# Optimization experiments

Measured on AMD Instinct MI355X. Metric: run time of the kernel, lower is better.

## Reference

```python
import jax, jax.numpy as jnp
import numpy as np

K = 3          # kernel size
KF = K * K     # kernel field = 9
PAD = 1
STRIDE = 1


def _conv(x, w, b):
    y = jax.lax.conv_general_dilated(
        x, w, (STRIDE, STRIDE), [(PAD, PAD), (PAD, PAD)],
        dimension_numbers=('NCHW', 'OIHW', 'NCHW'))
    return y + b[None, :, None, None]


def _bilinear_gather(x, py, px):
    # x: [B,C,H,W]; py/px: [B,KF,Ho,Wo] float sampling coords (zero-pad outside)
    B, C, H, W = x.shape
    xf = x.reshape(B, C, H * W)
    y0 = jnp.floor(py)
    x0 = jnp.floor(px)

    def corner(yc, xc):
        wy = 1.0 - jnp.abs(py - yc)
        wx = 1.0 - jnp.abs(px - xc)
        valid = (yc >= 0) & (yc <= H - 1) & (xc >= 0) & (xc <= W - 1)
        yi = jnp.clip(yc, 0, H - 1).astype(jnp.int32)
        xi = jnp.clip(xc, 0, W - 1).astype(jnp.int32)
        idx = (yi * W + xi).reshape(B, -1)               # [B, KF*Ho*Wo]
        v = jax.vmap(lambda f, i: f[:, i])(xf, idx)      # [B, C, KF*Ho*Wo]
        wgt = (wy * wx * valid.astype(x.dtype)).reshape(B, 1, -1)
        return v * wgt

    return (corner(y0, x0) + corner(y0, x0 + 1) +
            corner(y0 + 1, x0) + corner(y0 + 1, x0 + 1))  # [B,C,KF*Ho*Wo]


def _deform_conv(x, offset, mask, w, b):
    # modulated deformable conv v2 (mmcv offset layout: [y,x] interleaved per kernel pt)
    B, C, H, W = x.shape
    Ho, Wo = mask.shape[2], mask.shape[3]
    kh, kw = jnp.meshgrid(jnp.arange(K), jnp.arange(K), indexing='ij')
    kh = kh.reshape(-1).astype(x.dtype)   # [KF]
    kw = kw.reshape(-1).astype(x.dtype)
    base_y = (jnp.arange(Ho) * STRIDE - PAD).astype(x.dtype)
    base_x = (jnp.arange(Wo) * STRIDE - PAD).astype(x.dtype)
    off = offset.reshape(B, KF, 2, Ho, Wo)
    py = base_y[None, None, :, None] + kh[None, :, None, None] + off[:, :, 0]
    px = base_x[None, None, None, :] + kw[None, :, None, None] + off[:, :, 1]
    val = _bilinear_gather(x, py, px).reshape(B, C, KF, Ho, Wo)
    val = val * mask[:, None]                             # modulate
    out = jnp.einsum('bckhw,ock->bohw', val, w.reshape(w.shape[0], C, KF))
    return out + b[None, :, None, None]


def setup_inputs() -> dict:
    key = jax.random.key(0)
    k1, k2, k3 = jax.random.split(key, 3)
    B, C, H, W = 8, 64, 128, 128
    x = jax.random.normal(k1, (B, C, H, W), dtype=jnp.float32)
    w_om = jax.random.normal(k2, (3 * KF, C, K, K), dtype=jnp.float32) * 0.02
    b_om = jnp.zeros((3 * KF,), dtype=jnp.float32)
    w_dc = jax.random.normal(k3, (64, C, K, K), dtype=jnp.float32) * 0.05
    b_dc = jnp.zeros((64,), dtype=jnp.float32)
    return {"x": x, "w_om": w_om, "b_om": b_om, "w_dc": w_dc, "b_dc": b_dc}


def reference(x, w_om, b_om, w_dc, b_dc):
    om = _conv(x, w_om, b_om)                 # [B, 3*KF, H, W]
    offset = om[:, :2 * KF]
    mask = 2.0 * jax.nn.sigmoid(om[:, 2 * KF:])
    return _deform_conv(x, offset, mask, w_dc, b_dc)
```

## Files before the change

kernel.cpp:

```cpp
#include <hip/hip_runtime.h>
#include <cmath>

#define IH 128
#define IW 128
#define NB 8

typedef __attribute__((ext_vector_type(8))) short bf16x8;
typedef __attribute__((ext_vector_type(4))) float f32x4;

union U4B8 { uint4 u; bf16x8 h; };

#define OFFM_OFF 0
#define XT_OFF   3538944
#define WTDC_OFF (3538944 + 4194304)
#define WTOM_OFF (3538944 + 4194304 + 18432)

__device__ __forceinline__ unsigned short f32_to_bf16(float f) {
    unsigned int u = __float_as_uint(f);
    u += 0x7fffu + ((u >> 16) & 1u);
    return (unsigned short)(u >> 16);
}

__global__ void transpose_weights(const float* __restrict__ w_dc,
                                  const float* __restrict__ w_om,
                                  unsigned short* __restrict__ wt_dc16,
                                  unsigned short* __restrict__ wt_om16) {
    int idx = blockIdx.x * blockDim.x + threadIdx.x;
    if (idx < 9 * 64 * 64) {
        int k = idx >> 12;
        int o = (idx >> 6) & 63;
        int c = idx & 63;
        wt_dc16[idx] = f32_to_bf16(w_dc[(o * 64 + c) * 9 + k]);
    }
    if (idx < 9 * 32 * 64) {
        int k = idx >> 11;
        int o = (idx >> 6) & 31;
        int c = idx & 63;
        wt_om16[idx] = (o < 27) ? f32_to_bf16(w_om[(o * 64 + c) * 9 + k])
                                : (unsigned short)0;
    }
}

__global__ __launch_bounds__(256) void transpose_x(
        const float* __restrict__ x, unsigned short* __restrict__ xT) {
    __shared__ float t[64 * 65];
    const int tid = threadIdx.x;
    const int blk = blockIdx.x;
    const int b = blk >> 8;
    const int rem = blk & 255;
    const int h = rem >> 1;
    const int w0 = (rem & 1) << 6;

    for (int i = tid; i < 4096; i += 256) {
        const int c = i >> 6;
        const int w = i & 63;
        t[w * 65 + c] = x[(((size_t)(b * 64 + c)) << 14) + (h << 7) + w0 + w];
    }
    __syncthreads();
    const int c2 = (tid & 31) * 2;
    ushort2* dst = (ushort2*)(xT + (((size_t)b << 20)) + ((size_t)((h << 7) + w0)) * 64 + c2);
#pragma unroll
    for (int p = 0; p < 8; ++p) {
        const int w = (tid >> 5) + p * 8;
        ushort2 u;
        u.x = f32_to_bf16(t[w * 65 + c2]);
        u.y = f32_to_bf16(t[w * 65 + c2 + 1]);
        dst[(size_t)w * 32] = u;
    }
}

__global__ __launch_bounds__(256) void conv_om_mfma(
        const unsigned short* __restrict__ xT,
        const float* __restrict__ b_om,
        const unsigned short* __restrict__ wt_om16,
        float* __restrict__ offm) {
    __shared__ __align__(16) unsigned short win[198 * 72];
    __shared__ __align__(16) unsigned short wks[2][32 * 72];

    const int tid = threadIdx.x;
    const int b = blockIdx.x >> 8;
    const int rem = blockIdx.x & 255;
    const int h = rem >> 1;
    const int w0 = (rem & 1) << 6;
    const int wid = tid >> 6;
    const int lane = tid & 63;
    const int ln15 = lane & 15;
    const int quad = lane >> 4;

    for (int idx = tid; idx < 1584; idx += 256) {
        const int pos = idx >> 3;
        const int part = idx & 7;
        const int r = pos / 66;
        const int xx = pos - r * 66;
        const int y = h + r - 1;
        const int xg = w0 + xx - 1;
        uint4 v = make_uint4(0u, 0u, 0u, 0u);
        if (y >= 0 && y < IH && xg >= 0 && xg < IW)
            v = *(const uint4*)(xT + (((size_t)b << 20) + (((y << 7) + xg) << 6) + (part << 3)));
        *(uint4*)&win[pos * 72 + part * 8] = v;
    }
    {
        const int o = tid >> 3;
        const int part = tid & 7;
        *(uint4*)&wks[0][o * 72 + part * 8] =
            *(const uint4*)(wt_om16 + (o << 6) + (part << 3));
    }
    __syncthreads();

    f32x4 acc[2] = {{0.f, 0.f, 0.f, 0.f}, {0.f, 0.f, 0.f, 0.f}};

    for (int k = 0; k < 9; ++k) {
        const int buf = k & 1;
        if (k < 8) {
            const int o = tid >> 3;
            const int part = tid & 7;
            *(uint4*)&wks[buf ^ 1][o * 72 + part * 8] =
                *(const uint4*)(wt_om16 + ((k + 1) << 11) + (o << 6) + (part << 3));
        }
        const int kh = k / 3;
        const int kw = k - kh * 3;
        const int posb = kh * 66 + wid * 16 + ln15 + kw;
        const unsigned short* wb = wks[buf];
#pragma unroll
        for (int ch = 0; ch < 2; ++ch) {
            const int c = (ch << 5) + (quad << 3);
            U4B8 a, b0, b1;
            a.u  = *(const uint4*)&win[posb * 72 + c];
            b0.u = *(const uint4*)&wb[ln15 * 72 + c];
            b1.u = *(const uint4*)&wb[(16 + ln15) * 72 + c];
            acc[0] = __builtin_amdgcn_mfma_f32_16x16x32_bf16(a.h, b0.h, acc[0], 0, 0, 0);
            acc[1] = __builtin_amdgcn_mfma_f32_16x16x32_bf16(a.h, b1.h, acc[1], 0, 0, 0);
        }
        __syncthreads();
    }

    const int px0 = wid * 16 + quad * 4;
#pragma unroll
    for (int ot = 0; ot < 2; ++ot) {
        const int o = (ot << 4) + ln15;
        if (o >= 27) continue;
        const float bias = b_om[o];
        float4 r;
        r.x = acc[ot][0] + bias;
        r.y = acc[ot][1] + bias;
        r.z = acc[ot][2] + bias;
        r.w = acc[ot][3] + bias;
        if (o >= 18) {
            r.x = 2.0f / (1.0f + __expf(-r.x));
            r.y = 2.0f / (1.0f + __expf(-r.y));
            r.z = 2.0f / (1.0f + __expf(-r.z));
            r.w = 2.0f / (1.0f + __expf(-r.w));
        }
        *(float4*)&offm[(((size_t)(b * 27 + o)) << 14) + (h << 7) + w0 + px0] = r;
    }
}

__device__ __forceinline__ void corner2(const unsigned short* __restrict__ p,
                                        float wgt, float* v) {
    const uint4 a = *(const uint4*)p;
    const uint4 c = *(const uint4*)(p + 32);
    unsigned int u[8] = {a.x, a.y, a.z, a.w, c.x, c.y, c.z, c.w};
#pragma unroll
    for (int i = 0; i < 8; ++i) {
        v[2 * i]     += wgt * __uint_as_float(u[i] << 16);
        v[2 * i + 1] += wgt * __uint_as_float(u[i] & 0xffff0000u);
    }
}

__device__ __forceinline__ void gather_frags(
        const unsigned short* __restrict__ xb, const float* __restrict__ offs,
        int k, int lpx, int h, int w0, int quad, U4B8& a0, U4B8& a1) {
    const float offy = offs[(k << 1) * 64 + lpx];
    const float offx = offs[((k << 1) + 1) * 64 + lpx];
    const float msk  = offs[(18 + k) * 64 + lpx];
    const int kh = k / 3;
    const int kw = k - kh * 3;
    const float py  = (float)(h + kh - 1) + offy;
    const float pxf = (float)(w0 + lpx + kw - 1) + offx;
    const float y0f = floorf(py);
    const float x0f = floorf(pxf);
    const float fy = py - y0f;
    const float fx = pxf - x0f;
    const float wy0 = 1.0f - fy, wx0 = 1.0f - fx;
    const float vy0 = (y0f >= 0.0f && y0f <= 127.0f) ? 1.0f : 0.0f;
    const float vy1 = (y0f >= -1.0f && y0f <= 126.0f) ? 1.0f : 0.0f;
    const float vx0 = (x0f >= 0.0f && x0f <= 127.0f) ? 1.0f : 0.0f;
    const float vx1 = (x0f >= -1.0f && x0f <= 126.0f) ? 1.0f : 0.0f;
    const float w00 = wy0 * wx0 * vy0 * vx0;
    const float w01 = wy0 * fx  * vy0 * vx1;
    const float w10 = fy  * wx0 * vy1 * vx0;
    const float w11 = fy  * fx  * vy1 * vx1;
    const int y0i = min(max((int)y0f, 0), 127);
    const int y1i = min(max((int)y0f + 1, 0), 127);
    const int x0i = min(max((int)x0f, 0), 127);
    const int x1i = min(max((int)x0f + 1, 0), 127);

    float v[16];
#pragma unroll
    for (int i = 0; i < 16; ++i) v[i] = 0.0f;
    const int cofs = quad << 3;
    corner2(xb + ((((size_t)((y0i << 7) + x0i)) << 6) + cofs), w00, v);
    corner2(xb + ((((size_t)((y0i << 7) + x1i)) << 6) + cofs), w01, v);
    corner2(xb + ((((size_t)((y1i << 7) + x0i)) << 6) + cofs), w10, v);
    corner2(xb + ((((size_t)((y1i << 7) + x1i)) << 6) + cofs), w11, v);

    unsigned int pk[8];
#pragma unroll
    for (int i = 0; i < 8; ++i) {
        const unsigned int lo = f32_to_bf16(v[2 * i] * msk);
        const unsigned int hi = f32_to_bf16(v[2 * i + 1] * msk);
        pk[i] = lo | (hi << 16);
    }
    a0.u = make_uint4(pk[0], pk[1], pk[2], pk[3]);
    a1.u = make_uint4(pk[4], pk[5], pk[6], pk[7]);
}

__global__ __launch_bounds__(256) void deform_mfma(
        const unsigned short* __restrict__ xT,
        const float* __restrict__ b_dc,
        const float* __restrict__ offm,
        const unsigned short* __restrict__ wt_dc16,
        float* __restrict__ out) {
    __shared__ __align__(16) float offs[27 * 64];
    __shared__ __align__(16) unsigned short wks[2][64 * 72];

    const int tid = threadIdx.x;
    const int b = blockIdx.x >> 8;
    const int rem = blockIdx.x & 255;
    const int h = rem >> 1;
    const int w0 = (rem & 1) << 6;
    const int wid = tid >> 6;
    const int lane = tid & 63;
    const int ln15 = lane & 15;
    const int quad = lane >> 4;
    const int lpx = (wid << 4) + ln15;

    for (int i = tid; i < 1728; i += 256) {
        const int ch = i >> 6;
        const int px = i & 63;
        offs[i] = offm[(((size_t)(b * 27 + ch)) << 14) + (h << 7) + w0 + px];
    }
    for (int s = tid; s < 512; s += 256) {
        const int o = s >> 3;
        const int part = s & 7;
        *(uint4*)&wks[0][o * 72 + part * 8] =
            *(const uint4*)(wt_dc16 + (o << 6) + (part << 3));
    }
    __syncthreads();

    const unsigned short* xb = xT + ((size_t)b << 20);

    f32x4 acc[4];
#pragma unroll
    for (int i = 0; i < 4; ++i) acc[i] = (f32x4){0.f, 0.f, 0.f, 0.f};

    U4B8 a0c, a1c;
    gather_frags(xb, offs, 0, lpx, h, w0, quad, a0c, a1c);

    for (int k = 0; k < 9; ++k) {
        const int buf = k & 1;
        U4B8 a0n, a1n;
        a0n.u = make_uint4(0u, 0u, 0u, 0u);
        a1n.u = make_uint4(0u, 0u, 0u, 0u);
        if (k < 8) {
            for (int s = tid; s < 512; s += 256) {
                const int o = s >> 3;
                const int part = s & 7;
                *(uint4*)&wks[buf ^ 1][o * 72 + part * 8] =
                    *(const uint4*)(wt_dc16 + ((k + 1) << 12) + (o << 6) + (part << 3));
            }
            gather_frags(xb, offs, k + 1, lpx, h, w0, quad, a0n, a1n);
        }
        const unsigned short* wb = wks[buf];
#pragma unroll
        for (int ot = 0; ot < 4; ++ot) {
            U4B8 b0, b1;
            const unsigned short* base = &wb[((ot << 4) + ln15) * 72 + (quad << 3)];
            b0.u = *(const uint4*)base;
            b1.u = *(const uint4*)(base + 32);
            acc[ot] = __builtin_amdgcn_mfma_f32_16x16x32_bf16(a0c.h, b0.h, acc[ot], 0, 0, 0);
            acc[ot] = __builtin_amdgcn_mfma_f32_16x16x32_bf16(a1c.h, b1.h, acc[ot], 0, 0, 0);
        }
        __syncthreads();
        a0c = a0n;
        a1c = a1n;
    }

#pragma unroll
    for (int ot = 0; ot < 4; ++ot) {
        const int o = (ot << 4) + ln15;
        const float bias = b_dc[o];
        float4 r;
        r.x = acc[ot][0] + bias;
        r.y = acc[ot][1] + bias;
        r.z = acc[ot][2] + bias;
        r.w = acc[ot][3] + bias;
        *(float4*)&out[(((size_t)(b * 64 + o)) << 14) + (h << 7) + w0 + (wid << 4) + (quad << 2)] = r;
    }
}

extern "C" void kernel_launch(void* const* d_in, const int* in_sizes, int n_in,
                              void* d_out, int out_size, void* d_ws, size_t ws_size,
                              hipStream_t stream) {
    const float* x    = (const float*)d_in[0];
    const float* w_om = (const float*)d_in[1];
    const float* b_om = (const float*)d_in[2];
    const float* w_dc = (const float*)d_in[3];
    const float* b_dc = (const float*)d_in[4];
    float* out = (float*)d_out;
    float* ws  = (float*)d_ws;

    float* offm = ws + OFFM_OFF;
    unsigned short* xT      = (unsigned short*)(ws + XT_OFF);
    unsigned short* wt_dc16 = (unsigned short*)(ws + WTDC_OFF);
    unsigned short* wt_om16 = (unsigned short*)(ws + WTOM_OFF);

    const int n_blocks = NB * IH * (IW / 64);

    transpose_weights<<<144, 256, 0, stream>>>(w_dc, w_om, wt_dc16, wt_om16);
    transpose_x<<<NB * IH * 2, 256, 0, stream>>>(x, xT);
    conv_om_mfma<<<n_blocks, 256, 0, stream>>>(xT, b_om, wt_om16, offm);
    deform_mfma<<<n_blocks, 256, 0, stream>>>(xT, b_dc, offm, wt_dc16, out);
}
```

Baseline: 190.5 us.

## Read MFMA weight fragments directly from global memory, dropping LDS staging and barriers

Both the offset/mask conv kernel and the deformable conv kernel stop double-buffering weights through shared memory. Each lane now loads its B fragments straight from global (L1/L2-cached) weight arrays, which removes the per-tap __syncthreads and part of the LDS footprint. The deform kernel also gets a launch_bounds occupancy hint of 8 blocks. The trade-off is more global load traffic and latency per MFMA, in exchange for no barriers and potentially higher occupancy, while the register cap from the hint may cause spills.

Result: slower. 285.9 us (+50.1%).

```diff
diff --git a/kernel.cpp b/kernel.cpp
--- a/kernel.cpp
+++ b/kernel.cpp
@@ -75,7 +75,6 @@
         const unsigned short* __restrict__ wt_om16,
         float* __restrict__ offm) {
     __shared__ __align__(16) unsigned short win[198 * 72];
-    __shared__ __align__(16) unsigned short wks[2][32 * 72];
 
     const int tid = threadIdx.x;
     const int b = blockIdx.x >> 8;
@@ -99,39 +98,25 @@
             v = *(const uint4*)(xT + (((size_t)b << 20) + (((y << 7) + xg) << 6) + (part << 3)));
         *(uint4*)&win[pos * 72 + part * 8] = v;
     }
-    {
-        const int o = tid >> 3;
-        const int part = tid & 7;
-        *(uint4*)&wks[0][o * 72 + part * 8] =
-            *(const uint4*)(wt_om16 + (o << 6) + (part << 3));
-    }
     __syncthreads();
 
     f32x4 acc[2] = {{0.f, 0.f, 0.f, 0.f}, {0.f, 0.f, 0.f, 0.f}};
 
     for (int k = 0; k < 9; ++k) {
-        const int buf = k & 1;
-        if (k < 8) {
-            const int o = tid >> 3;
-            const int part = tid & 7;
-            *(uint4*)&wks[buf ^ 1][o * 72 + part * 8] =
-                *(const uint4*)(wt_om16 + ((k + 1) << 11) + (o << 6) + (part << 3));
-        }
         const int kh = k / 3;
         const int kw = k - kh * 3;
         const int posb = kh * 66 + wid * 16 + ln15 + kw;
-        const unsigned short* wb = wks[buf];
+        const unsigned short* wg = wt_om16 + (k << 11);
 #pragma unroll
         for (int ch = 0; ch < 2; ++ch) {
             const int c = (ch << 5) + (quad << 3);
             U4B8 a, b0, b1;
             a.u  = *(const uint4*)&win[posb * 72 + c];
-            b0.u = *(const uint4*)&wb[ln15 * 72 + c];
-            b1.u = *(const uint4*)&wb[(16 + ln15) * 72 + c];
+            b0.u = *(const uint4*)(wg + (ln15 << 6) + c);
+            b1.u = *(const uint4*)(wg + ((16 + ln15) << 6) + c);
             acc[0] = __builtin_amdgcn_mfma_f32_16x16x32_bf16(a.h, b0.h, acc[0], 0, 0, 0);
             acc[1] = __builtin_amdgcn_mfma_f32_16x16x32_bf16(a.h, b1.h, acc[1], 0, 0, 0);
         }
-        __syncthreads();
     }
 
     const int px0 = wid * 16 + quad * 4;
@@ -215,14 +200,13 @@
     a1.u = make_uint4(pk[4], pk[5], pk[6], pk[7]);
 }
 
-__global__ __launch_bounds__(256) void deform_mfma(
+__global__ __launch_bounds__(256, 8) void deform_mfma(
         const unsigned short* __restrict__ xT,
         const float* __restrict__ b_dc,
         const float* __restrict__ offm,
         const unsigned short* __restrict__ wt_dc16,
         float* __restrict__ out) {
     __shared__ __align__(16) float offs[27 * 64];
-    __shared__ __align__(16) unsigned short wks[2][64 * 72];
 
     const int tid = threadIdx.x;
     const int b = blockIdx.x >> 8;
@@ -240,12 +224,6 @@
         const int px = i & 63;
         offs[i] = offm[(((size_t)(b * 27 + ch)) << 14) + (h << 7) + w0 + px];
     }
-    for (int s = tid; s < 512; s += 256) {
-        const int o = s >> 3;
-        const int part = s & 7;
-        *(uint4*)&wks[0][o * 72 + part * 8] =
-            *(const uint4*)(wt_dc16 + (o << 6) + (part << 3));
-    }
     __syncthreads();
 
     const unsigned short* xb = xT + ((size_t)b << 20);
@@ -258,30 +236,22 @@
     gather_frags(xb, offs, 0, lpx, h, w0, quad, a0c, a1c);
 
     for (int k = 0; k < 9; ++k) {
-        const int buf = k & 1;
         U4B8 a0n, a1n;
         a0n.u = make_uint4(0u, 0u, 0u, 0u);
         a1n.u = make_uint4(0u, 0u, 0u, 0u);
         if (k < 8) {
-            for (int s = tid; s < 512; s += 256) {
-                const int o = s >> 3;
-                const int part = s & 7;
-                *(uint4*)&wks[buf ^ 1][o * 72 + part * 8] =
-                    *(const uint4*)(wt_dc16 + ((k + 1) << 12) + (o << 6) + (part << 3));
-            }
             gather_frags(xb, offs, k + 1, lpx, h, w0, quad, a0n, a1n);
         }
-        const unsigned short* wb = wks[buf];
+        const unsigned short* wg = wt_dc16 + (k << 12);
 #pragma unroll
         for (int ot = 0; ot < 4; ++ot) {
             U4B8 b0, b1;
-            const unsigned short* base = &wb[((ot << 4) + ln15) * 72 + (quad << 3)];
+            const unsigned short* base = wg + (((ot << 4) + ln15) << 6) + (quad << 3);
             b0.u = *(const uint4*)base;
             b1.u = *(const uint4*)(base + 32);
             acc[ot] = __builtin_amdgcn_mfma_f32_16x16x32_bf16(a0c.h, b0.h, acc[ot], 0, 0, 0);
             acc[ot] = __builtin_amdgcn_mfma_f32_16x16x32_bf16(a1c.h, b1.h, acc[ot], 0, 0, 0);
         }
-        __syncthreads();
         a0c = a0n;
         a1c = a1n;
     }
```
